# Performance work log

Hardware: AMD Instinct MI355X
Metric: run time of the kernel (lower is better)

Reference implementation:

```python
import jax, jax.numpy as jnp
import numpy as np

# Dimensions: B graphs of NPG nodes each (equal sizes -> padding == reshape, exact)
B, NPG, DIN, H, E, DOUT, K_ORDER = 8, 4096, 128, 4, 262144, 128, 4
BETA = 0.5
N = B * NPG


def setup_inputs() -> dict:
    key = jax.random.key(0)
    k = jax.random.split(key, 12)
    s = 1.0 / np.sqrt(DIN)
    so = 1.0 / np.sqrt(H * DIN)
    x = jax.random.normal(k[0], (N, DIN), jnp.float32)
    Wq_w = jax.random.normal(k[1], (H * DIN, DIN), jnp.float32) * s
    Wq_b = jax.random.normal(k[2], (H * DIN,), jnp.float32) * 0.01
    Wk_w = jax.random.normal(k[3], (H * DIN, DIN), jnp.float32) * s
    Wk_b = jax.random.normal(k[4], (H * DIN,), jnp.float32) * 0.01
    Wo_w = jax.random.normal(k[5], (DOUT, H * DIN), jnp.float32) * so
    Wo_b = jax.random.normal(k[6], (DOUT,), jnp.float32) * 0.01
    # edges constrained within graphs (faithful to per-graph data)
    g = jax.random.randint(k[7], (E,), 0, B)
    row = g * NPG + jax.random.randint(k[8], (E,), 0, NPG)
    col = g * NPG + jax.random.randint(k[9], (E,), 0, NPG)
    edge_index = jnp.stack([row, col]).astype(jnp.int32)
    n_nodes = jnp.full((B,), NPG, jnp.int32)
    return {"x": x, "Wq_w": Wq_w, "Wq_b": Wq_b, "Wk_w": Wk_w, "Wk_b": Wk_b,
            "Wo_w": Wo_w, "Wo_b": Wo_b, "edge_index": edge_index, "n_nodes": n_nodes}


def _gcn(x, row, col):
    # x: [N,H,D]; symmetric-normalized message passing via segment sums
    deg = jax.ops.segment_sum(jnp.ones(row.shape[0], x.dtype), row, num_segments=N)
    safe = jnp.where(deg > 0, deg, 1.0)
    dis = jnp.where(deg > 0, safe ** -0.5, 0.0)
    w = (dis[row] * dis[col])[:, None, None]
    return jax.ops.segment_sum(x[col] * w, row, num_segments=N)


def _attn(qs, ks, v, n_f):
    # linear attention: out_i = (q_i . sum_j k_j v_j^T + sum_j v_j) / (q_i . sum_j k_j + n)
    q4 = qs.reshape(B, NPG, H, DIN)
    k4 = ks.reshape(B, NPG, H, DIN)
    v4 = v.reshape(B, NPG, H, DIN)
    kv = jnp.einsum('bnhd,bnhe->bhde', k4, v4)          # [B,H,D,D]
    ksum = k4.sum(axis=1)                                # [B,H,D]
    vsum = v4.sum(axis=1)                                # [B,H,D]
    num = jnp.einsum('bnhd,bhde->bnhe', q4, kv) + vsum[:, None]
    den = jnp.einsum('bnhd,bhd->bnh', q4, ksum) + n_f[:, None, None]
    return (num / den[..., None]).reshape(N, H, DIN)


def reference(x, Wq_w, Wq_b, Wk_w, Wk_b, Wo_w, Wo_b, edge_index, n_nodes):
    row, col = edge_index[0], edge_index[1]
    q = (x @ Wq_w.T + Wq_b).reshape(N, H, DIN)
    k = (x @ Wk_w.T + Wk_b).reshape(N, H, DIN)
    qs = q / jnp.linalg.norm(q, axis=2, keepdims=True)
    ks = k / jnp.linalg.norm(k, axis=2, keepdims=True)
    n_f = n_nodes.astype(x.dtype)
    xh = jnp.broadcast_to(x[:, None, :], (N, H, DIN))    # repeat over heads
    acc = xh
    cur = xh
    for _ in range(K_ORDER):
        cur = BETA * _gcn(cur, row, col) + (1.0 - BETA) * _attn(qs, ks, cur, n_f)
        acc = acc + cur
    xo = acc.reshape(N, H * DIN)
    return (xo @ Wo_w.T + Wo_b) / H
```

## Files before the change

kernel.cpp:

```cpp
#include <hip/hip_runtime.h>
#include <hip/hip_bf16.h>
#include <stdint.h>

typedef __hip_bfloat16 bf16;

#define BATCH  8
#define NPG    4096
#define DIN    128
#define NH     4
#define NEDGE  262144
#define DOUTF  128
#define KORDER 4
#define NTOT   (BATCH*NPG)
#define HD     (NH*DIN)

typedef __attribute__((ext_vector_type(8))) short short8;
typedef __attribute__((ext_vector_type(4))) float f32x4;

static __device__ __forceinline__ float b2f(bf16 v) { return __bfloat162float(v); }
static __device__ __forceinline__ float u2f(unsigned short u) {
    union { float f; unsigned int i; } c; c.i = ((unsigned int)u) << 16; return c.f;
}
static __device__ __forceinline__ unsigned short f2u(float f) {
    bf16 hb = __float2bfloat16(f);
    return *(unsigned short*)&hb;
}

__global__ void zero_kernel(uint4* p, int n) {
    int i = blockIdx.x * 256 + threadIdx.x;
    if (i < n) p[i] = uint4{0u, 0u, 0u, 0u};
}

__global__ void cvtbf_kernel(const float* __restrict__ in, bf16* __restrict__ out, int n) {
    int i = (blockIdx.x * 256 + threadIdx.x) * 8;
    if (i < n) {
        float4 a = *(const float4*)(in + i);
        float4 b = *(const float4*)(in + i + 4);
        unsigned short u[8] = { f2u(a.x), f2u(a.y), f2u(a.z), f2u(a.w),
                                f2u(b.x), f2u(b.y), f2u(b.z), f2u(b.w) };
        *(uint4*)(out + i) = *(uint4*)u;
    }
}

__global__ __launch_bounds__(256) void proj_mfma_kernel(const bf16* __restrict__ xbf,
                                                        const bf16* __restrict__ Wbf,
                                                        const float* __restrict__ bias,
                                                        bf16* __restrict__ outp,
                                                        bf16* __restrict__ outT) {
    __shared__ __align__(16) short t1[32][520];
    int n0 = blockIdx.x * 32;
    int tid = threadIdx.x;
    int lane = tid & 63, wc = tid >> 6;
    int l15 = lane & 15, quad = lane >> 4;

    f32x4 acc[2][8];
    #pragma unroll
    for (int i = 0; i < 2; i++)
        #pragma unroll
        for (int j = 0; j < 8; j++) acc[i][j] = f32x4{0.f, 0.f, 0.f, 0.f};

    #pragma unroll
    for (int ks = 0; ks < 4; ks++) {
        int kk = ks * 32 + quad * 8;
        short8 af[2];
        #pragma unroll
        for (int ti = 0; ti < 2; ti++)
            af[ti] = *(const short8*)(xbf + (size_t)(n0 + ti * 16 + l15) * DIN + kk);
        #pragma unroll
        for (int tj = 0; tj < 8; tj++) {
            short8 bfr = *(const short8*)(Wbf + (size_t)(wc * 128 + tj * 16 + l15) * DIN + kk);
            acc[0][tj] = __builtin_amdgcn_mfma_f32_16x16x32_bf16(af[0], bfr, acc[0][tj], 0, 0, 0);
            acc[1][tj] = __builtin_amdgcn_mfma_f32_16x16x32_bf16(af[1], bfr, acc[1][tj], 0, 0, 0);
        }
    }

    float bias_v[8];
    #pragma unroll
    for (int tj = 0; tj < 8; tj++) bias_v[tj] = bias[wc * 128 + tj * 16 + l15];

    #pragma unroll
    for (int ti = 0; ti < 2; ti++) {
        #pragma unroll
        for (int r = 0; r < 4; r++) {
            float s = 0.f;
            #pragma unroll
            for (int tj = 0; tj < 8; tj++) {
                float v = acc[ti][tj][r] + bias_v[tj];
                acc[ti][tj][r] = v;
                s += v * v;
            }
            s += __shfl_xor(s, 1); s += __shfl_xor(s, 2);
            s += __shfl_xor(s, 4); s += __shfl_xor(s, 8);
            float rs = rsqrtf(s);
            int node = ti * 16 + quad * 4 + r;
            #pragma unroll
            for (int tj = 0; tj < 8; tj++)
                t1[node][wc * 128 + tj * 16 + l15] = (short)f2u(acc[ti][tj][r] * rs);
        }
    }
    __syncthreads();

    if (outp) {
        #pragma unroll
        for (int u = 0; u < 8; u++) {
            int unit = u * 256 + tid;
            int nl = unit >> 6, fp = (unit & 63) * 8;
            *(uint4*)(outp + (size_t)(n0 + nl) * HD + fp) = *(uint4*)&t1[nl][fp];
        }
    }
    if (outT) {
        int b = n0 >> 12, nl0 = n0 & 4095;
        #pragma unroll
        for (int u = 0; u < 8; u++) {
            int unit = u * 256 + tid;
            int f = unit >> 2, np = (unit & 3) * 8;
            unsigned short arr[8];
            #pragma unroll
            for (int j = 0; j < 8; j++) arr[j] = (unsigned short)t1[np + j][f];
            *(uint4*)(outT + ((size_t)b * HD + f) * NPG + nl0 + np) = *(uint4*)arr;
        }
    }
}

__global__ void deg_kernel(const int* __restrict__ row, int* __restrict__ deg) {
    int e = blockIdx.x * 256 + threadIdx.x;
    if (e < NEDGE) atomicAdd(&deg[row[e]], 1);
}

__global__ void dis_kernel(const int* __restrict__ deg, float* __restrict__ dis) {
    int i = blockIdx.x * 256 + threadIdx.x;
    if (i < NTOT) {
        int d = deg[i];
        dis[i] = d > 0 ? rsqrtf((float)d) : 0.f;
    }
}

__global__ __launch_bounds__(1024) void scan1_kernel(const int* __restrict__ deg,
                                                     int* __restrict__ row_ptr, int* __restrict__ bsum) {
    __shared__ int buf[1024];
    int g = blockIdx.x, t = threadIdx.x;
    int v = deg[g * 1024 + t];
    buf[t] = v;
    __syncthreads();
    for (int off = 1; off < 1024; off <<= 1) {
        int add = (t >= off) ? buf[t - off] : 0;
        __syncthreads();
        buf[t] += add;
        __syncthreads();
    }
    row_ptr[g * 1024 + t] = buf[t] - v;
    if (t == 1023) bsum[g] = buf[1023];
}

__global__ void scan2_kernel(const int* __restrict__ bsum, int* __restrict__ boff, int* __restrict__ row_ptr) {
    int run = 0;
    for (int g = 0; g < 32; g++) { boff[g] = run; run += bsum[g]; }
    row_ptr[NTOT] = run;
}

__global__ __launch_bounds__(1024) void scan3_kernel(int* __restrict__ row_ptr, const int* __restrict__ boff) {
    row_ptr[blockIdx.x * 1024 + threadIdx.x] += boff[blockIdx.x];
}

__global__ void scatter_kernel(const int* __restrict__ row, const int* __restrict__ col,
                               const int* __restrict__ row_ptr, int* __restrict__ fill,
                               const float* __restrict__ dis,
                               uint2* __restrict__ ecw) {
    int e = blockIdx.x * 256 + threadIdx.x;
    if (e < NEDGE) {
        int r = row[e], c = col[e];
        int pos = row_ptr[r] + atomicAdd(&fill[r], 1);
        ecw[pos] = uint2{(unsigned)c, __float_as_uint(dis[c])};
    }
}

__global__ __launch_bounds__(256) void rowsum_kernel(const bf16* __restrict__ T, float* __restrict__ out) {
    int row = blockIdx.x * 4 + (threadIdx.x >> 6);
    int lane = threadIdx.x & 63;
    const ushort4* p = (const ushort4*)(T + (size_t)row * NPG);
    float s = 0.f;
    #pragma unroll
    for (int wv = 0; wv < 16; wv++) {
        ushort4 u = p[lane + wv * 64];
        s += u2f(u.x) + u2f(u.y) + u2f(u.z) + u2f(u.w);
    }
    for (int off = 32; off > 0; off >>= 1) s += __shfl_down(s, off);
    if (lane == 0) out[row] = s;
}

__global__ __launch_bounds__(256) void den_kernel(const bf16* __restrict__ qs, const float* __restrict__ ksum,
                                                  const int* __restrict__ n_nodes, float* __restrict__ rden) {
    int n = blockIdx.x;
    int b = n >> 12;
    int w = threadIdx.x >> 6, lane = threadIdx.x & 63;
    int base = w * DIN;
    float p = b2f(qs[(size_t)n * HD + base + lane])      * ksum[b * HD + base + lane]
            + b2f(qs[(size_t)n * HD + base + 64 + lane]) * ksum[b * HD + base + 64 + lane];
    for (int off = 32; off > 0; off >>= 1) p += __shfl_down(p, off);
    if (lane == 0) rden[n * NH + w] = 1.0f / (p + (float)n_nodes[b]);
}

__global__ __launch_bounds__(512) void init_kernel(const bf16* __restrict__ xbf, bf16* __restrict__ cur,
                                                   bf16* __restrict__ curT, bf16* __restrict__ acc) {
    int node0 = blockIdx.x * 8;
    int t = threadIdx.x;
    int d = t & 127;
    int b = node0 >> 12, nl = node0 & 4095;
    unsigned short arr[8];
    #pragma unroll
    for (int r = 0; r < 8; r++) {
        bf16 hb = xbf[(size_t)(node0 + r) * DIN + d];
        cur[(size_t)(node0 + r) * HD + t] = hb;
        acc[(size_t)(node0 + r) * HD + t] = hb;
        arr[r] = *(unsigned short*)&hb;
    }
    *(uint4*)(curT + ((size_t)b * HD + t) * NPG + nl) = *(uint4*)arr;
}

#define KVSPLIT 8
__global__ __launch_bounds__(512, 1) void kv_mfma_kernel(const bf16* __restrict__ ksT,
                                                         const bf16* __restrict__ curT,
                                                         float* __restrict__ partial) {
    __shared__ __align__(16) short kshT[128][72];
    __shared__ __align__(16) short vshT[128][72];
    int id = blockIdx.x;
    int b = id & 7;
    int u = id >> 3;
    int h = u >> 3;
    int s = u & 7;
    int bh = b * 4 + h;
    int blk = bh * KVSPLIT + s;
    int tid = threadIdx.x;
    int lane = tid & 63;
    int w = tid >> 6;
    int wr = w >> 1, wc = w & 1;
    int d0w = wr * 32, e0w = wc * 64;
    int l15 = lane & 15, quad = lane >> 4;

    f32x4 acc[2][4];
    #pragma unroll
    for (int i = 0; i < 2; i++)
        #pragma unroll
        for (int j = 0; j < 4; j++) acc[i][j] = f32x4{0.f, 0.f, 0.f, 0.f};

    const uint4* kg = (const uint4*)(ksT + ((size_t)bh * 128) * NPG);
    const uint4* vg = (const uint4*)(curT + ((size_t)bh * 128) * NPG);
    int n0 = s * (NPG / KVSPLIT);

    for (int c = 0; c < 8; c++) {
        int nb = n0 + c * 64;
        #pragma unroll
        for (int uu = 0; uu < 2; uu++) {
            int unit = uu * 512 + tid;
            int row = unit >> 3;
            int part = unit & 7;
            int gidx = row * (NPG / 8) + (nb >> 3) + part;
            uint4 kd = kg[gidx];
            uint4 vd = vg[gidx];
            *(uint4*)&kshT[row][part * 8] = kd;
            *(uint4*)&vshT[row][part * 8] = vd;
        }
        __syncthreads();
        #pragma unroll
        for (int kkstep = 0; kkstep < 2; kkstep++) {
            int kk = kkstep * 32 + quad * 8;
            short8 af[2], bfr[4];
            #pragma unroll
            for (int ti = 0; ti < 2; ti++)
                af[ti] = *(const short8*)&kshT[d0w + ti * 16 + l15][kk];
            #pragma unroll
            for (int tj = 0; tj < 4; tj++)
                bfr[tj] = *(const short8*)&vshT[e0w + tj * 16 + l15][kk];
            #pragma unroll
            for (int ti = 0; ti < 2; ti++)
                #pragma unroll
                for (int tj = 0; tj < 4; tj++)
                    acc[ti][tj] = __builtin_amdgcn_mfma_f32_16x16x32_bf16(af[ti], bfr[tj], acc[ti][tj], 0, 0, 0);
        }
        __syncthreads();
    }
    float* p = partial + (size_t)blk * (128 * 128);
    #pragma unroll
    for (int ti = 0; ti < 2; ti++)
        #pragma unroll
        for (int tj = 0; tj < 4; tj++)
            #pragma unroll
            for (int r = 0; r < 4; r++) {
                int row = d0w + ti * 16 + quad * 4 + r;
                int col = e0w + tj * 16 + l15;
                p[row * 128 + col] = acc[ti][tj][r];
            }
}

__global__ __launch_bounds__(256) void kvredB_kernel(const float* __restrict__ partial, bf16* __restrict__ kvB) {
    __shared__ __align__(16) short t[16][136];
    int blk = blockIdx.x;
    int bh = blk >> 3;
    int e0 = (blk & 7) * 16;
    int tid = threadIdx.x;
    int el = tid & 15;
    int dc = tid >> 4;
    const float* p = partial + (size_t)bh * (KVSPLIT * 16384);
    #pragma unroll
    for (int j = 0; j < 8; j++) {
        int d = dc * 8 + j;
        int idx = d * 128 + e0 + el;
        float s = 0.f;
        #pragma unroll
        for (int sl = 0; sl < KVSPLIT; sl++) s += p[sl * 16384 + idx];
        t[el][d] = (short)f2u(s);
    }
    __syncthreads();
    int e = tid >> 4, dp = (tid & 15) * 8;
    *(uint4*)((unsigned short*)kvB + (size_t)bh * 16384 + (e0 + e) * 128 + dp) = *(uint4*)&t[e][dp];
}

static __device__ __forceinline__ void acc8(float* g, uint4 v, float w) {
    unsigned short* sv = (unsigned short*)&v;
    #pragma unroll
    for (int k = 0; k < 8; k++) g[k] += w * u2f(sv[k]);
}

#define EMAX 1536
__global__ __launch_bounds__(512, 2) void gcn_attn_kernel(const bf16* __restrict__ qs,
                                                          const bf16* __restrict__ kvB,
                                                          const bf16* __restrict__ cur,
                                                          const int* __restrict__ row_ptr,
                                                          const uint2* __restrict__ ecw,
                                                          const float* __restrict__ dis,
                                                          const float* __restrict__ vsum,
                                                          const float* __restrict__ rden,
                                                          bf16* __restrict__ curN,
                                                          bf16* __restrict__ curTN,
                                                          bf16* __restrict__ accb,
                                                          float* __restrict__ vsumN) {
    __shared__ __align__(16) short t1[128][136];
    __shared__ __align__(8) uint2 est[EMAX];
    int id = blockIdx.x;
    int b = id & 7;
    int u = id >> 3;
    int h = u >> 5;
    int m = u & 31;
    int bh = b * 4 + h;
    int n0 = b * NPG + m * 128;
    int tid = threadIdx.x;
    int lane = tid & 63, w = tid >> 6;
    int wr = w >> 1, wc = w & 1;
    int e0w = wc * 64;
    int l15 = lane & 15, quad = lane >> 4;

    int ebase = row_ptr[n0];
    int ecnt = row_ptr[n0 + 128] - ebase;
    int scnt = ecnt < EMAX ? ecnt : EMAX;
    for (int i = tid; i < scnt; i += 512) est[i] = ecw[ebase + i];
    __syncthreads();

    {
        int nl = tid >> 2;
        int sub = tid & 3;
        int n = n0 + nl;
        int start = row_ptr[n] - ebase;
        int end   = row_ptr[n + 1] - ebase;
        int lend  = end < scnt ? end : scnt;
        float g[32];
        #pragma unroll
        for (int i = 0; i < 32; i++) g[i] = 0.f;
        const bf16* gbase = cur + (size_t)h * DIN + sub * 32;

        int cA = 0, cB = 0; float wA = 0.f, wB = 0.f;
        if (start < lend)     { uint2 p = est[start];     cA = (int)p.x; wA = __uint_as_float(p.y); }
        if (start + 1 < lend) { uint2 p = est[start + 1]; cB = (int)p.x; wB = __uint_as_float(p.y); }
        uint4 vA0, vA1, vA2, vA3, vB0, vB1, vB2, vB3;
        {
            const uint4* p = (const uint4*)(gbase + (size_t)cA * HD);
            vA0 = p[0]; vA1 = p[1]; vA2 = p[2]; vA3 = p[3];
        }
        {
            const uint4* p = (const uint4*)(gbase + (size_t)cB * HD);
            vB0 = p[0]; vB1 = p[1]; vB2 = p[2]; vB3 = p[3];
        }
        for (int j = start; j < lend; j += 2) {
            int cC = 0, cD = 0; float wC = 0.f, wD = 0.f;
            if (j + 2 < lend) { uint2 p = est[j + 2]; cC = (int)p.x; wC = __uint_as_float(p.y); }
            if (j + 3 < lend) { uint2 p = est[j + 3]; cD = (int)p.x; wD = __uint_as_float(p.y); }
            acc8(g +  0, vA0, wA); acc8(g +  8, vA1, wA);
            acc8(g + 16, vA2, wA); acc8(g + 24, vA3, wA);
            {
                const uint4* p = (const uint4*)(gbase + (size_t)cC * HD);
                vA0 = p[0]; vA1 = p[1]; vA2 = p[2]; vA3 = p[3];
            }
            acc8(g +  0, vB0, wB); acc8(g +  8, vB1, wB);
            acc8(g + 16, vB2, wB); acc8(g + 24, vB3, wB);
            {
                const uint4* p = (const uint4*)(gbase + (size_t)cD * HD);
                vB0 = p[0]; vB1 = p[1]; vB2 = p[2]; vB3 = p[3];
            }
            wA = wC; wB = wD;
        }
        int fstart = start > lend ? start : lend;
        for (int j = fstart; j < end; j++) {
            uint2 pe = ecw[ebase + j];
            int c = (int)pe.x; float ww = __uint_as_float(pe.y);
            const uint4* p = (const uint4*)(gbase + (size_t)c * HD);
            acc8(g +  0, p[0], ww); acc8(g +  8, p[1], ww);
            acc8(g + 16, p[2], ww); acc8(g + 24, p[3], ww);
        }

        float dn = dis[n];
        int sw = (nl >> 3) & 7;
        #pragma unroll
        for (int q = 0; q < 4; q++) {
            unsigned short arr[8];
            #pragma unroll
            for (int k = 0; k < 8; k++) arr[k] = f2u(g[q * 8 + k] * dn);
            int fb = (sub * 4 + q) ^ sw;
            *(uint4*)&t1[nl][fb * 8] = *(uint4*)arr;
        }
    }

    f32x4 acc[2][4];
    #pragma unroll
    for (int i = 0; i < 2; i++)
        #pragma unroll
        for (int j = 0; j < 4; j++) acc[i][j] = f32x4{0.f, 0.f, 0.f, 0.f};

    const bf16* Aq = qs + (size_t)n0 * HD + h * DIN;
    const unsigned short* Bk = (const unsigned short*)kvB + (size_t)bh * 16384;
    #pragma unroll
    for (int ks = 0; ks < 4; ks++) {
        int kk = ks * 32 + quad * 8;
        short8 af[2], bfr[4];
        #pragma unroll
        for (int ti = 0; ti < 2; ti++)
            af[ti] = *(const short8*)(Aq + (size_t)(wr * 32 + ti * 16 + l15) * HD + kk);
        #pragma unroll
        for (int tj = 0; tj < 4; tj++)
            bfr[tj] = *(const short8*)(Bk + (e0w + tj * 16 + l15) * 128 + kk);
        #pragma unroll
        for (int ti = 0; ti < 2; ti++)
            #pragma unroll
            for (int tj = 0; tj < 4; tj++)
                acc[ti][tj] = __builtin_amdgcn_mfma_f32_16x16x32_bf16(af[ti], bfr[tj], acc[ti][tj], 0, 0, 0);
    }
    __syncthreads();

    #pragma unroll
    for (int tj = 0; tj < 4; tj++) {
        int el = e0w + tj * 16 + l15;
        float vs = vsum[b * HD + h * DIN + el];
        float cs = 0.f;
        #pragma unroll
        for (int ti = 0; ti < 2; ti++) {
            int nlb = wr * 32 + ti * 16 + quad * 4;
            #pragma unroll
            for (int r = 0; r < 4; r++) {
                int nl = nlb + r;
                int sw = (nl >> 3) & 7;
                int pc = (((el >> 3) ^ sw) * 8) | (el & 7);
                float attnv = (acc[ti][tj][r] + vs) * rden[(size_t)(n0 + nl) * NH + h];
                float g = u2f((unsigned short)t1[nl][pc]);
                float val = 0.5f * g + 0.5f * attnv;
                t1[nl][pc] = (short)f2u(val);
                cs += val;
            }
        }
        cs += __shfl_xor(cs, 16);
        cs += __shfl_xor(cs, 32);
        if (quad == 0) atomicAdd(&vsumN[b * HD + h * DIN + el], cs);
    }
    __syncthreads();

    {
        bf16* dstn = curN + (size_t)n0 * HD + h * DIN;
        bf16* dsta = accb + (size_t)n0 * HD + h * DIN;
        #pragma unroll
        for (int uu = 0; uu < 4; uu++) {
            int unit = uu * 512 + tid;
            int nl = unit >> 4, fb = unit & 15;
            int sw = (nl >> 3) & 7;
            uint4 v = *(uint4*)&t1[nl][(fb ^ sw) * 8];
            *(uint4*)(dstn + (size_t)nl * HD + fb * 8) = v;
            unsigned short* sv = (unsigned short*)&v;
            unsigned short* ap = (unsigned short*)(dsta + (size_t)nl * HD + fb * 8);
            uint4 a = *(uint4*)ap;
            unsigned short* av = (unsigned short*)&a;
            unsigned short res[8];
            #pragma unroll
            for (int j = 0; j < 8; j++) res[j] = f2u(u2f(av[j]) + u2f(sv[j]));
            *(uint4*)ap = *(uint4*)res;
        }
    }
    {
        bf16* dstT = curTN + ((size_t)b * HD + h * DIN) * NPG + m * 128;
        #pragma unroll
        for (int uu = 0; uu < 4; uu++) {
            int unit = uu * 512 + tid;
            int fl = unit >> 4, np = (unit & 15) * 8;
            unsigned short arr[8];
            #pragma unroll
            for (int j = 0; j < 8; j++) {
                int row = np + j;
                int sw = (row >> 3) & 7;
                int pc = (((fl >> 3) ^ sw) * 8) | (fl & 7);
                arr[j] = (unsigned short)t1[row][pc];
            }
            *(uint4*)(dstT + (size_t)fl * NPG + np) = *(uint4*)arr;
        }
    }
}

__global__ __launch_bounds__(512) void out_mfma_kernel(const bf16* __restrict__ accb,
                                                       const bf16* __restrict__ Wobf,
                                                       const float* __restrict__ Wo_b,
                                                       float* __restrict__ out) {
    int n0 = blockIdx.x * 128;
    int tid = threadIdx.x;
    int lane = tid & 63, w = tid >> 6;
    int wr = w >> 1, wc = w & 1;
    int l15 = lane & 15, quad = lane >> 4;

    f32x4 acc[2][4];
    #pragma unroll
    for (int i = 0; i < 2; i++)
        #pragma unroll
        for (int j = 0; j < 4; j++) acc[i][j] = f32x4{0.f, 0.f, 0.f, 0.f};

    for (int ks = 0; ks < 16; ks++) {
        int kk = ks * 32 + quad * 8;
        short8 af[2], bfr[4];
        #pragma unroll
        for (int ti = 0; ti < 2; ti++)
            af[ti] = *(const short8*)(accb + (size_t)(n0 + wr * 32 + ti * 16 + l15) * HD + kk);
        #pragma unroll
        for (int tj = 0; tj < 4; tj++)
            bfr[tj] = *(const short8*)(Wobf + (size_t)(wc * 64 + tj * 16 + l15) * HD + kk);
        #pragma unroll
        for (int ti = 0; ti < 2; ti++)
            #pragma unroll
            for (int tj = 0; tj < 4; tj++)
                acc[ti][tj] = __builtin_amdgcn_mfma_f32_16x16x32_bf16(af[ti], bfr[tj], acc[ti][tj], 0, 0, 0);
    }

    #pragma unroll
    for (int tj = 0; tj < 4; tj++) {
        int col = wc * 64 + tj * 16 + l15;
        float bv = Wo_b[col];
        #pragma unroll
        for (int ti = 0; ti < 2; ti++) {
            int rowb = wr * 32 + ti * 16 + quad * 4;
            #pragma unroll
            for (int r = 0; r < 4; r++)
                out[(size_t)(n0 + rowb + r) * DOUTF + col] = (acc[ti][tj][r] + bv) * 0.25f;
        }
    }
}

extern "C" void kernel_launch(void* const* d_in, const int* in_sizes, int n_in,
                              void* d_out, int out_size, void* d_ws, size_t ws_size,
                              hipStream_t stream) {
    const float* x     = (const float*)d_in[0];
    const float* Wq_w  = (const float*)d_in[1];
    const float* Wq_b  = (const float*)d_in[2];
    const float* Wk_w  = (const float*)d_in[3];
    const float* Wk_b  = (const float*)d_in[4];
    const float* Wo_w  = (const float*)d_in[5];
    const float* Wo_b  = (const float*)d_in[6];
    const int*   edge  = (const int*)d_in[7];
    const int*   n_nod = (const int*)d_in[8];
    float* out = (float*)d_out;
    const int* erow = edge;
    const int* ecol = edge + NEDGE;

    char* w = (char*)d_ws;
    auto alloc = [&](size_t bytes) -> char* {
        char* p = w;
        w += (bytes + 255) & ~(size_t)255;
        return p;
    };
    bf16*  qs      = (bf16*) alloc((size_t)NTOT * HD * 2);
    bf16*  ksT     = (bf16*) alloc((size_t)NTOT * HD * 2);
    bf16*  curA    = (bf16*) alloc((size_t)NTOT * HD * 2);
    bf16*  curB    = (bf16*) alloc((size_t)NTOT * HD * 2);
    bf16*  curTA   = (bf16*) alloc((size_t)NTOT * HD * 2);
    bf16*  curTB   = (bf16*) alloc((size_t)NTOT * HD * 2);
    bf16*  accb    = (bf16*) alloc((size_t)NTOT * HD * 2);
    float* partial = (float*)alloc((size_t)32 * KVSPLIT * 16384 * 4);
    bf16*  kvB     = (bf16*) alloc((size_t)32 * 16384 * 2);
    bf16*  Wobf    = (bf16*) alloc(DOUTF * HD * 2);
    int*   degfill = (int*)  alloc(2 * NTOT * 4);
    float* dis     = (float*)alloc(NTOT * 4);
    int*   row_ptr = (int*)  alloc((NTOT + 1) * 4);
    uint2* ecw     = (uint2*)alloc((size_t)NEDGE * 8);
    float* ksum    = (float*)alloc(BATCH * HD * 4);
    float* vsumA   = (float*)alloc(BATCH * HD * 4);
    float* vsumB   = (float*)alloc(BATCH * HD * 4);
    float* rden    = (float*)alloc((size_t)NTOT * NH * 4);
    int*   bsum    = (int*)  alloc(32 * 4);
    int*   boff    = (int*)  alloc(32 * 4);
    int* deg  = degfill;
    int* fill = degfill + NTOT;
    bf16* xbf  = (bf16*)partial;
    bf16* Wqbf = (bf16*)((char*)partial + (8 << 20));
    bf16* Wkbf = Wqbf + (size_t)HD * DIN;

    zero_kernel<<<64, 256, 0, stream>>>((uint4*)degfill, 2 * NTOT / 4);

    cvtbf_kernel<<<NTOT * DIN / 8 / 256, 256, 0, stream>>>(x, xbf, NTOT * DIN);
    cvtbf_kernel<<<HD * DIN / 8 / 256, 256, 0, stream>>>(Wq_w, Wqbf, HD * DIN);
    cvtbf_kernel<<<HD * DIN / 8 / 256, 256, 0, stream>>>(Wk_w, Wkbf, HD * DIN);
    cvtbf_kernel<<<DOUTF * HD / 8 / 256, 256, 0, stream>>>(Wo_w, Wobf, DOUTF * HD);

    proj_mfma_kernel<<<NTOT / 32, 256, 0, stream>>>(xbf, Wqbf, Wq_b, qs, (bf16*)nullptr);
    proj_mfma_kernel<<<NTOT / 32, 256, 0, stream>>>(xbf, Wkbf, Wk_b, (bf16*)nullptr, ksT);

    deg_kernel<<<NEDGE / 256, 256, 0, stream>>>(erow, deg);
    dis_kernel<<<NTOT / 256, 256, 0, stream>>>(deg, dis);
    scan1_kernel<<<32, 1024, 0, stream>>>(deg, row_ptr, bsum);
    scan2_kernel<<<1, 1, 0, stream>>>(bsum, boff, row_ptr);
    scan3_kernel<<<32, 1024, 0, stream>>>(row_ptr, boff);
    scatter_kernel<<<NEDGE / 256, 256, 0, stream>>>(erow, ecol, row_ptr, fill, dis, ecw);

    rowsum_kernel<<<BATCH * HD / 4, 256, 0, stream>>>(ksT, ksum);
    den_kernel<<<NTOT, 256, 0, stream>>>(qs, ksum, n_nod, rden);

    init_kernel<<<NTOT / 8, 512, 0, stream>>>(xbf, curA, curTA, accb);
    rowsum_kernel<<<BATCH * HD / 4, 256, 0, stream>>>(curTA, vsumA);

    bf16* c = curA;  bf16* cT = curTA;
    bf16* cn = curB; bf16* cnT = curTB;
    float* vs = vsumA;
    float* vsN = vsumB;
    for (int it = 0; it < KORDER; it++) {
        kv_mfma_kernel<<<32 * KVSPLIT, 512, 0, stream>>>(ksT, cT, partial);
        kvredB_kernel<<<256, 256, 0, stream>>>(partial, kvB);
        zero_kernel<<<4, 256, 0, stream>>>((uint4*)vsN, BATCH * HD / 4);
        gcn_attn_kernel<<<32 * 32, 512, 0, stream>>>(qs, kvB, c, row_ptr, ecw, dis,
                                                     vs, rden, cn, cnT, accb, vsN);
        bf16* t;
        t = c; c = cn; cn = t;
        t = cT; cT = cnT; cnT = t;
        float* tf = vs; vs = vsN; vsN = tf;
    }

    out_mfma_kernel<<<NTOT / 128, 512, 0, stream>>>(accb, Wobf, Wo_b, out);

    (void)in_sizes; (void)n_in; (void)out_size; (void)ws_size;
}
```

Measured before the change: 608.8 us.

## Drop transposed cur and accumulator buffers, keep per-order outputs and sum in output GEMM

Each propagation step now keeps its own node-major output buffer. The step no longer writes a transposed copy or does a read-modify-write of the bf16 accumulator. The KV GEMM loads V directly from node-major data and transposes it into swizzled shared memory, while the first step reads x directly with a zero head stride, so the init kernel is removed. The output GEMM sums x and the four step outputs on the fly, which saves global traffic in the hot loop but adds five loads per operand fragment in the final GEMM and scattered LDS stores in the KV kernel.

Result: faster. 579.3 us (-4.8%).

```diff
diff --git a/kernel.cpp b/kernel.cpp
--- a/kernel.cpp
+++ b/kernel.cpp
@@ -188,6 +188,23 @@
     if (lane == 0) out[row] = s;
 }
 
+__global__ __launch_bounds__(256) void colsum_kernel(const bf16* __restrict__ xbf, float* __restrict__ vsum) {
+    __shared__ float buf[256];
+    int b = blockIdx.x >> 3, sl = blockIdx.x & 7;
+    int t = threadIdx.x;
+    int d = t & 127, half = t >> 7;
+    const unsigned short* p = (const unsigned short*)xbf + ((size_t)b * NPG + sl * 512 + half * 256) * DIN + d;
+    float s = 0.f;
+    for (int r = 0; r < 256; r++) s += u2f(p[(size_t)r * DIN]);
+    buf[t] = s;
+    __syncthreads();
+    if (half == 0) {
+        float tot = buf[d] + buf[d + 128];
+        #pragma unroll
+        for (int h = 0; h < NH; h++) atomicAdd(&vsum[b * HD + h * DIN + d], tot);
+    }
+}
+
 __global__ __launch_bounds__(256) void den_kernel(const bf16* __restrict__ qs, const float* __restrict__ ksum,
                                                   const int* __restrict__ n_nodes, float* __restrict__ rden) {
     int n = blockIdx.x;
@@ -200,26 +217,10 @@
     if (lane == 0) rden[n * NH + w] = 1.0f / (p + (float)n_nodes[b]);
 }
 
-__global__ __launch_bounds__(512) void init_kernel(const bf16* __restrict__ xbf, bf16* __restrict__ cur,
-                                                   bf16* __restrict__ curT, bf16* __restrict__ acc) {
-    int node0 = blockIdx.x * 8;
-    int t = threadIdx.x;
-    int d = t & 127;
-    int b = node0 >> 12, nl = node0 & 4095;
-    unsigned short arr[8];
-    #pragma unroll
-    for (int r = 0; r < 8; r++) {
-        bf16 hb = xbf[(size_t)(node0 + r) * DIN + d];
-        cur[(size_t)(node0 + r) * HD + t] = hb;
-        acc[(size_t)(node0 + r) * HD + t] = hb;
-        arr[r] = *(unsigned short*)&hb;
-    }
-    *(uint4*)(curT + ((size_t)b * HD + t) * NPG + nl) = *(uint4*)arr;
-}
-
 #define KVSPLIT 8
 __global__ __launch_bounds__(512, 1) void kv_mfma_kernel(const bf16* __restrict__ ksT,
-                                                         const bf16* __restrict__ curT,
+                                                         const bf16* __restrict__ vsrc,
+                                                         int vld, int vhm,
                                                          float* __restrict__ partial) {
     __shared__ __align__(16) short kshT[128][72];
     __shared__ __align__(16) short vshT[128][72];
@@ -244,7 +245,7 @@
         for (int j = 0; j < 4; j++) acc[i][j] = f32x4{0.f, 0.f, 0.f, 0.f};
 
     const uint4* kg = (const uint4*)(ksT + ((size_t)bh * 128) * NPG);
-    const uint4* vg = (const uint4*)(curT + ((size_t)bh * 128) * NPG);
+    const bf16* vg = vsrc + (size_t)h * vhm;
     int n0 = s * (NPG / KVSPLIT);
 
     for (int c = 0; c < 8; c++) {
@@ -254,11 +255,15 @@
             int unit = uu * 512 + tid;
             int row = unit >> 3;
             int part = unit & 7;
-            int gidx = row * (NPG / 8) + (nb >> 3) + part;
-            uint4 kd = kg[gidx];
-            uint4 vd = vg[gidx];
+            uint4 kd = kg[row * (NPG / 8) + (nb >> 3) + part];
             *(uint4*)&kshT[row][part * 8] = kd;
-            *(uint4*)&vshT[row][part * 8] = vd;
+            int nl = unit >> 4;
+            int fg = unit & 15;
+            uint4 vd = *(const uint4*)(vg + (size_t)(b * NPG + nb + nl) * vld + fg * 8);
+            unsigned short* sv = (unsigned short*)&vd;
+            int ncol = nl ^ ((fg & 7) << 3);
+            #pragma unroll
+            for (int j = 0; j < 8; j++) vshT[fg * 8 + j][ncol] = (short)sv[j];
         }
         __syncthreads();
         #pragma unroll
@@ -269,8 +274,10 @@
             for (int ti = 0; ti < 2; ti++)
                 af[ti] = *(const short8*)&kshT[d0w + ti * 16 + l15][kk];
             #pragma unroll
-            for (int tj = 0; tj < 4; tj++)
-                bfr[tj] = *(const short8*)&vshT[e0w + tj * 16 + l15][kk];
+            for (int tj = 0; tj < 4; tj++) {
+                int e = e0w + tj * 16 + l15;
+                bfr[tj] = *(const short8*)&vshT[e][kk ^ (((e >> 3) & 7) << 3)];
+            }
             #pragma unroll
             for (int ti = 0; ti < 2; ti++)
                 #pragma unroll
@@ -324,15 +331,14 @@
 #define EMAX 1536
 __global__ __launch_bounds__(512, 2) void gcn_attn_kernel(const bf16* __restrict__ qs,
                                                           const bf16* __restrict__ kvB,
-                                                          const bf16* __restrict__ cur,
+                                                          const bf16* __restrict__ gsrc,
+                                                          int gld, int ghm,
                                                           const int* __restrict__ row_ptr,
                                                           const uint2* __restrict__ ecw,
                                                           const float* __restrict__ dis,
                                                           const float* __restrict__ vsum,
                                                           const float* __restrict__ rden,
                                                           bf16* __restrict__ curN,
-                                                          bf16* __restrict__ curTN,
-                                                          bf16* __restrict__ accb,
                                                           float* __restrict__ vsumN) {
     __shared__ __align__(16) short t1[128][136];
     __shared__ __align__(8) uint2 est[EMAX];
@@ -365,18 +371,18 @@
         float g[32];
         #pragma unroll
         for (int i = 0; i < 32; i++) g[i] = 0.f;
-        const bf16* gbase = cur + (size_t)h * DIN + sub * 32;
+        const bf16* gbase = gsrc + (size_t)h * ghm + sub * 32;
 
         int cA = 0, cB = 0; float wA = 0.f, wB = 0.f;
         if (start < lend)     { uint2 p = est[start];     cA = (int)p.x; wA = __uint_as_float(p.y); }
         if (start + 1 < lend) { uint2 p = est[start + 1]; cB = (int)p.x; wB = __uint_as_float(p.y); }
         uint4 vA0, vA1, vA2, vA3, vB0, vB1, vB2, vB3;
         {
-            const uint4* p = (const uint4*)(gbase + (size_t)cA * HD);
+            const uint4* p = (const uint4*)(gbase + (size_t)cA * gld);
             vA0 = p[0]; vA1 = p[1]; vA2 = p[2]; vA3 = p[3];
         }
         {
-            const uint4* p = (const uint4*)(gbase + (size_t)cB * HD);
+            const uint4* p = (const uint4*)(gbase + (size_t)cB * gld);
             vB0 = p[0]; vB1 = p[1]; vB2 = p[2]; vB3 = p[3];
         }
         for (int j = start; j < lend; j += 2) {
@@ -386,13 +392,13 @@
             acc8(g +  0, vA0, wA); acc8(g +  8, vA1, wA);
             acc8(g + 16, vA2, wA); acc8(g + 24, vA3, wA);
             {
-                const uint4* p = (const uint4*)(gbase + (size_t)cC * HD);
+                const uint4* p = (const uint4*)(gbase + (size_t)cC * gld);
                 vA0 = p[0]; vA1 = p[1]; vA2 = p[2]; vA3 = p[3];
             }
             acc8(g +  0, vB0, wB); acc8(g +  8, vB1, wB);
             acc8(g + 16, vB2, wB); acc8(g + 24, vB3, wB);
             {
-                const uint4* p = (const uint4*)(gbase + (size_t)cD * HD);
+                const uint4* p = (const uint4*)(gbase + (size_t)cD * gld);
                 vB0 = p[0]; vB1 = p[1]; vB2 = p[2]; vB3 = p[3];
             }
             wA = wC; wB = wD;
@@ -401,7 +407,7 @@
         for (int j = fstart; j < end; j++) {
             uint2 pe = ecw[ebase + j];
             int c = (int)pe.x; float ww = __uint_as_float(pe.y);
-            const uint4* p = (const uint4*)(gbase + (size_t)c * HD);
+            const uint4* p = (const uint4*)(gbase + (size_t)c * gld);
             acc8(g +  0, p[0], ww); acc8(g +  8, p[1], ww);
             acc8(g + 16, p[2], ww); acc8(g + 24, p[3], ww);
         }
@@ -472,7 +478,6 @@
 
     {
         bf16* dstn = curN + (size_t)n0 * HD + h * DIN;
-        bf16* dsta = accb + (size_t)n0 * HD + h * DIN;
         #pragma unroll
         for (int uu = 0; uu < 4; uu++) {
             int unit = uu * 512 + tid;
@@ -480,36 +485,15 @@
             int sw = (nl >> 3) & 7;
             uint4 v = *(uint4*)&t1[nl][(fb ^ sw) * 8];
             *(uint4*)(dstn + (size_t)nl * HD + fb * 8) = v;
-            unsigned short* sv = (unsigned short*)&v;
-            unsigned short* ap = (unsigned short*)(dsta + (size_t)nl * HD + fb * 8);
-            uint4 a = *(uint4*)ap;
-            unsigned short* av = (unsigned short*)&a;
-            unsigned short res[8];
-            #pragma unroll
-            for (int j = 0; j < 8; j++) res[j] = f2u(u2f(av[j]) + u2f(sv[j]));
-            *(uint4*)ap = *(uint4*)res;
-        }
-    }
-    {
-        bf16* dstT = curTN + ((size_t)b * HD + h * DIN) * NPG + m * 128;
-        #pragma unroll
-        for (int uu = 0; uu < 4; uu++) {
-            int unit = uu * 512 + tid;
-            int fl = unit >> 4, np = (unit & 15) * 8;
-            unsigned short arr[8];
-            #pragma unroll
-            for (int j = 0; j < 8; j++) {
-                int row = np + j;
-                int sw = (row >> 3) & 7;
-                int pc = (((fl >> 3) ^ sw) * 8) | (fl & 7);
-                arr[j] = (unsigned short)t1[row][pc];
-            }
-            *(uint4*)(dstT + (size_t)fl * NPG + np) = *(uint4*)arr;
-        }
-    }
-}
-
-__global__ __launch_bounds__(512) void out_mfma_kernel(const bf16* __restrict__ accb,
+        }
+    }
+}
+
+__global__ __launch_bounds__(512) void out_mfma_kernel(const bf16* __restrict__ xbf,
+                                                       const bf16* __restrict__ c1,
+                                                       const bf16* __restrict__ c2,
+                                                       const bf16* __restrict__ c3,
+                                                       const bf16* __restrict__ c4,
                                                        const bf16* __restrict__ Wobf,
                                                        const float* __restrict__ Wo_b,
                                                        float* __restrict__ out) {
@@ -527,10 +511,27 @@
 
     for (int ks = 0; ks < 16; ks++) {
         int kk = ks * 32 + quad * 8;
+        int d = kk & 127;
         short8 af[2], bfr[4];
         #pragma unroll
-        for (int ti = 0; ti < 2; ti++)
-            af[ti] = *(const short8*)(accb + (size_t)(n0 + wr * 32 + ti * 16 + l15) * HD + kk);
+        for (int ti = 0; ti < 2; ti++) {
+            int row = n0 + wr * 32 + ti * 16 + l15;
+            uint4 vx = *(const uint4*)(xbf + (size_t)row * DIN + d);
+            uint4 v1 = *(const uint4*)(c1 + (size_t)row * HD + kk);
+            uint4 v2 = *(const uint4*)(c2 + (size_t)row * HD + kk);
+            uint4 v3 = *(const uint4*)(c3 + (size_t)row * HD + kk);
+            uint4 v4 = *(const uint4*)(c4 + (size_t)row * HD + kk);
+            unsigned short* px = (unsigned short*)&vx;
+            unsigned short* p1 = (unsigned short*)&v1;
+            unsigned short* p2 = (unsigned short*)&v2;
+            unsigned short* p3 = (unsigned short*)&v3;
+            unsigned short* p4 = (unsigned short*)&v4;
+            unsigned short o[8];
+            #pragma unroll
+            for (int j = 0; j < 8; j++)
+                o[j] = f2u(u2f(px[j]) + u2f(p1[j]) + u2f(p2[j]) + u2f(p3[j]) + u2f(p4[j]));
+            af[ti] = *(short8*)o;
+        }
         #pragma unroll
         for (int tj = 0; tj < 4; tj++)
             bfr[tj] = *(const short8*)(Wobf + (size_t)(wc * 64 + tj * 16 + l15) * HD + kk);
@@ -579,11 +580,11 @@
     };
     bf16*  qs      = (bf16*) alloc((size_t)NTOT * HD * 2);
     bf16*  ksT     = (bf16*) alloc((size_t)NTOT * HD * 2);
-    bf16*  curA    = (bf16*) alloc((size_t)NTOT * HD * 2);
-    bf16*  curB    = (bf16*) alloc((size_t)NTOT * HD * 2);
-    bf16*  curTA   = (bf16*) alloc((size_t)NTOT * HD * 2);
-    bf16*  curTB   = (bf16*) alloc((size_t)NTOT * HD * 2);
-    bf16*  accb    = (bf16*) alloc((size_t)NTOT * HD * 2);
+    bf16*  cur1    = (bf16*) alloc((size_t)NTOT * HD * 2);
+    bf16*  cur2    = (bf16*) alloc((size_t)NTOT * HD * 2);
+    bf16*  cur3    = (bf16*) alloc((size_t)NTOT * HD * 2);
+    bf16*  cur4    = (bf16*) alloc((size_t)NTOT * HD * 2);
+    bf16*  xbf     = (bf16*) alloc((size_t)NTOT * DIN * 2);
     float* partial = (float*)alloc((size_t)32 * KVSPLIT * 16384 * 4);
     bf16*  kvB     = (bf16*) alloc((size_t)32 * 16384 * 2);
     bf16*  Wobf    = (bf16*) alloc(DOUTF * HD * 2);
@@ -599,8 +600,7 @@
     int*   boff    = (int*)  alloc(32 * 4);
     int* deg  = degfill;
     int* fill = degfill + NTOT;
-    bf16* xbf  = (bf16*)partial;
-    bf16* Wqbf = (bf16*)((char*)partial + (8 << 20));
+    bf16* Wqbf = (bf16*)partial;
     bf16* Wkbf = Wqbf + (size_t)HD * DIN;
 
     zero_kernel<<<64, 256, 0, stream>>>((uint4*)degfill, 2 * NTOT / 4);
@@ -623,26 +623,25 @@
     rowsum_kernel<<<BATCH * HD / 4, 256, 0, stream>>>(ksT, ksum);
     den_kernel<<<NTOT, 256, 0, stream>>>(qs, ksum, n_nod, rden);
 
-    init_kernel<<<NTOT / 8, 512, 0, stream>>>(xbf, curA, curTA, accb);
-    rowsum_kernel<<<BATCH * HD / 4, 256, 0, stream>>>(curTA, vsumA);
-
-    bf16* c = curA;  bf16* cT = curTA;
-    bf16* cn = curB; bf16* cnT = curTB;
+    zero_kernel<<<4, 256, 0, stream>>>((uint4*)vsumA, BATCH * HD / 4);
+    colsum_kernel<<<64, 256, 0, stream>>>(xbf, vsumA);
+
+    bf16* curs[4] = { cur1, cur2, cur3, cur4 };
     float* vs = vsumA;
     float* vsN = vsumB;
     for (int it = 0; it < KORDER; it++) {
-        kv_mfma_kernel<<<32 * KVSPLIT, 512, 0, stream>>>(ksT, cT, partial);
+        const bf16* src = (it == 0) ? xbf : curs[it - 1];
+        int ld = (it == 0) ? DIN : HD;
+        int hm = (it == 0) ? 0 : DIN;
+        kv_mfma_kernel<<<32 * KVSPLIT, 512, 0, stream>>>(ksT, src, ld, hm, partial);
         kvredB_kernel<<<256, 256, 0, stream>>>(partial, kvB);
         zero_kernel<<<4, 256, 0, stream>>>((uint4*)vsN, BATCH * HD / 4);
-        gcn_attn_kernel<<<32 * 32, 512, 0, stream>>>(qs, kvB, c, row_ptr, ecw, dis,
-                                                     vs, rden, cn, cnT, accb, vsN);
-        bf16* t;
-        t = c; c = cn; cn = t;
-        t = cT; cT = cnT; cnT = t;
+        gcn_attn_kernel<<<32 * 32, 512, 0, stream>>>(qs, kvB, src, ld, hm, row_ptr, ecw, dis,
+                                                     vs, rden, curs[it], vsN);
         float* tf = vs; vs = vsN; vsN = tf;
     }
 
-    out_mfma_kernel<<<NTOT / 128, 512, 0, stream>>>(accb, Wobf, Wo_b, out);
+    out_mfma_kernel<<<NTOT / 128, 512, 0, stream>>>(xbf, cur1, cur2, cur3, cur4, Wobf, Wo_b, out);
 
     (void)in_sizes; (void)n_in; (void)out_size; (void)ws_size;
 }
```
